# Performance work log

Measured on AMD Instinct MI355X. Metric: run time of the kernel, lower is better.

## Reference

```python
import jax, jax.numpy as jnp
import numpy as np

N_ROWS = 4_194_304  # batch rows
N_LAYERS = 30


def setup_inputs() -> dict:
    key = jax.random.key(0)
    k1, k2, k3, k4, k5 = jax.random.split(key, 5)
    x1 = jax.random.normal(k1, (N_ROWS, 1), dtype=jnp.float32)
    x2 = jax.random.normal(k2, (N_ROWS, 5), dtype=jnp.float32)
    # Per-layer params stacked: Linear(5->1) weight [1,5] + bias [1]; Linear(1->5, no bias) weight [5,1]
    W1 = jax.random.normal(k3, (N_LAYERS, 1, 5), dtype=jnp.float32) * (1.0 / np.sqrt(5.0))
    b1 = jax.random.normal(k4, (N_LAYERS, 1), dtype=jnp.float32) * (1.0 / np.sqrt(5.0))
    W2 = jax.random.normal(k5, (N_LAYERS, 5, 1), dtype=jnp.float32)
    return {"x1": x1, "x2": x2, "W1": W1, "b1": b1, "W2": W2}


def reference(x1, x2, W1, b1, W2):
    # Chain of 30 UpDownDoubleResNetBlock blocks:
    #   x1 = x1 + relu(x2) @ W1^T + b1   (Linear(5,1) with bias)
    #   x2 = x2 + relu(x1) @ W2^T        (Linear(1,5) no bias)
    def step(carry, params):
        h1, h2 = carry
        w1, bb1, w2 = params  # [1,5], [1], [5,1]
        h1 = h1 + jax.nn.relu(h2) @ w1.T + bb1  # [N,1]
        h2 = h2 + jax.nn.relu(h1) @ w2.T        # [N,5]
        return (h1, h2), None

    (x1, x2), _ = jax.lax.scan(step, (x1, x2), (W1, b1, W2))
    return (x1, x2)
```

## Files before the change

### kernel.cpp

```cpp
#include <hip/hip_runtime.h>

#define NL 30
#define RPB 512

typedef float v2f __attribute__((ext_vector_type(2)));

__global__ __launch_bounds__(256) void drn_kernel(
    const float* __restrict__ x1, const float* __restrict__ x2,
    const float* __restrict__ W1, const float* __restrict__ b1,
    const float* __restrict__ W2,
    float* __restrict__ o1, float* __restrict__ o2)
{
    __shared__ __align__(16) float slab[RPB * 5];

    const int t = threadIdx.x;
    const int base = blockIdx.x * RPB;

    const v2f* g2 = (const v2f*)(x2 + (size_t)base * 5);
    v2f* s2 = (v2f*)slab;
    #pragma unroll
    for (int k = 0; k < 5; ++k)
        s2[t + 256 * k] = g2[t + 256 * k];

    float h1x = x1[base + t];
    float h1y = x1[base + 256 + t];

    __syncthreads();

    float h2x[5], h2y[5];
    #pragma unroll
    for (int j = 0; j < 5; ++j) {
        h2x[j] = slab[5 * t + j];
        h2y[j] = slab[5 * t + 1280 + j];
    }

    #pragma unroll
    for (int l = 0; l < NL; ++l) {
        const float w10 = W1[l * 5 + 0], w11 = W1[l * 5 + 1], w12 = W1[l * 5 + 2],
                    w13 = W1[l * 5 + 3], w14 = W1[l * 5 + 4];
        const float bb  = b1[l];
        const float w20 = W2[l * 5 + 0], w21 = W2[l * 5 + 1], w22 = W2[l * 5 + 2],
                    w23 = W2[l * 5 + 3], w24 = W2[l * 5 + 4];

        {
            float s = h1x + bb;
            s = fmaf(fmaxf(h2x[0], 0.f), w10, s);
            s = fmaf(fmaxf(h2x[1], 0.f), w11, s);
            s = fmaf(fmaxf(h2x[2], 0.f), w12, s);
            s = fmaf(fmaxf(h2x[3], 0.f), w13, s);
            s = fmaf(fmaxf(h2x[4], 0.f), w14, s);
            h1x = s;
            const float rh = fmaxf(s, 0.f);
            h2x[0] = fmaf(rh, w20, h2x[0]);
            h2x[1] = fmaf(rh, w21, h2x[1]);
            h2x[2] = fmaf(rh, w22, h2x[2]);
            h2x[3] = fmaf(rh, w23, h2x[3]);
            h2x[4] = fmaf(rh, w24, h2x[4]);
        }
        {
            float s = h1y + bb;
            s = fmaf(fmaxf(h2y[0], 0.f), w10, s);
            s = fmaf(fmaxf(h2y[1], 0.f), w11, s);
            s = fmaf(fmaxf(h2y[2], 0.f), w12, s);
            s = fmaf(fmaxf(h2y[3], 0.f), w13, s);
            s = fmaf(fmaxf(h2y[4], 0.f), w14, s);
            h1y = s;
            const float rh = fmaxf(s, 0.f);
            h2y[0] = fmaf(rh, w20, h2y[0]);
            h2y[1] = fmaf(rh, w21, h2y[1]);
            h2y[2] = fmaf(rh, w22, h2y[2]);
            h2y[3] = fmaf(rh, w23, h2y[3]);
            h2y[4] = fmaf(rh, w24, h2y[4]);
        }
    }

    __builtin_nontemporal_store(h1x, &o1[base + t]);
    __builtin_nontemporal_store(h1y, &o1[base + 256 + t]);

    __syncthreads();
    #pragma unroll
    for (int j = 0; j < 5; ++j) {
        slab[5 * t + j]        = h2x[j];
        slab[5 * t + 1280 + j] = h2y[j];
    }
    __syncthreads();
    v2f* go2 = (v2f*)(o2 + (size_t)base * 5);
    #pragma unroll
    for (int k = 0; k < 5; ++k)
        __builtin_nontemporal_store(s2[t + 256 * k], &go2[t + 256 * k]);
}

extern "C" void kernel_launch(void* const* d_in, const int* in_sizes, int n_in,
                              void* d_out, int out_size, void* d_ws, size_t ws_size,
                              hipStream_t stream) {
    const float* x1 = (const float*)d_in[0];
    const float* x2 = (const float*)d_in[1];
    const float* W1 = (const float*)d_in[2];
    const float* b1 = (const float*)d_in[3];
    const float* W2 = (const float*)d_in[4];
    int nrows = in_sizes[0];
    float* o1 = (float*)d_out;
    float* o2 = (float*)d_out + nrows;

    int block = 256;
    int grid = nrows / RPB;
    drn_kernel<<<grid, block, 0, stream>>>(x1, x2, W1, b1, W2, o1, o2);
}
```

Before: 188.8 us.

## Use persistent per-wave tiles with register prefetch of the next tile

Replaces one-shot 512-row blocks with a fixed grid of 2048 blocks in which each wave owns a private LDS section and loops over 128-row tiles. The next tile's x1/x2 loads are issued into registers before the current tile's 30-layer compute, so global load latency overlaps the arithmetic, and block-wide __syncthreads is dropped in favour of wave-local compiler fences. This trades more register pressure and reliance on intra-wave LDS ordering for fewer block launches and better latency hiding.

```diff
diff --git a/kernel.cpp b/kernel.cpp
--- a/kernel.cpp
+++ b/kernel.cpp
@@ -1,93 +1,119 @@
 #include <hip/hip_runtime.h>
 
 #define NL 30
-#define RPB 512
+#define NBLK 2048
+#define NWAVES (NBLK * 4)
 
 typedef float v2f __attribute__((ext_vector_type(2)));
 
-__global__ __launch_bounds__(256) void drn_kernel(
+#define LDS_FENCE() asm volatile("" ::: "memory")
+
+__global__ __launch_bounds__(256, 8) void drn_kernel(
     const float* __restrict__ x1, const float* __restrict__ x2,
     const float* __restrict__ W1, const float* __restrict__ b1,
     const float* __restrict__ W2,
-    float* __restrict__ o1, float* __restrict__ o2)
+    float* __restrict__ o1, float* __restrict__ o2, int ntiles)
 {
-    __shared__ __align__(16) float slab[RPB * 5];
+    __shared__ __align__(16) float slab[4 * 640];
 
-    const int t = threadIdx.x;
-    const int base = blockIdx.x * RPB;
+    const int lane = threadIdx.x & 63;
+    const int w    = threadIdx.x >> 6;
+    float* sect  = &slab[w * 640];
+    v2f*   sect2 = (v2f*)sect;
 
-    const v2f* g2 = (const v2f*)(x2 + (size_t)base * 5);
-    v2f* s2 = (v2f*)slab;
+    const v2f* g2  = (const v2f*)x2;
+    v2f*       go2 = (v2f*)o2;
+
+    int tile = blockIdx.x * 4 + w;
+    if (tile >= ntiles) return;
+
+    v2f L[5];
     #pragma unroll
-    for (int k = 0; k < 5; ++k)
-        s2[t + 256 * k] = g2[t + 256 * k];
+    for (int k = 0; k < 5; ++k) L[k] = g2[(size_t)tile * 320 + lane + 64 * k];
+    float h1xn = x1[tile * 128 + lane];
+    float h1yn = x1[tile * 128 + 64 + lane];
 
-    float h1x = x1[base + t];
-    float h1y = x1[base + 256 + t];
+    while (true) {
+        LDS_FENCE();
+        #pragma unroll
+        for (int k = 0; k < 5; ++k) sect2[lane + 64 * k] = L[k];
+        const float h1x0 = h1xn, h1y0 = h1yn;
 
-    __syncthreads();
+        LDS_FENCE();
+        float h2x[5], h2y[5];
+        #pragma unroll
+        for (int j = 0; j < 5; ++j) {
+            h2x[j] = sect[5 * lane + j];
+            h2y[j] = sect[320 + 5 * lane + j];
+        }
 
-    float h2x[5], h2y[5];
-    #pragma unroll
-    for (int j = 0; j < 5; ++j) {
-        h2x[j] = slab[5 * t + j];
-        h2y[j] = slab[5 * t + 1280 + j];
+        const int ntile = tile + NWAVES;
+        const bool have_next = ntile < ntiles;
+        if (have_next) {
+            #pragma unroll
+            for (int k = 0; k < 5; ++k) L[k] = g2[(size_t)ntile * 320 + lane + 64 * k];
+            h1xn = x1[ntile * 128 + lane];
+            h1yn = x1[ntile * 128 + 64 + lane];
+        }
+
+        float h1x = h1x0, h1y = h1y0;
+        #pragma unroll
+        for (int l = 0; l < NL; ++l) {
+            const float w10 = W1[l*5+0], w11 = W1[l*5+1], w12 = W1[l*5+2],
+                        w13 = W1[l*5+3], w14 = W1[l*5+4];
+            const float bb  = b1[l];
+            const float w20 = W2[l*5+0], w21 = W2[l*5+1], w22 = W2[l*5+2],
+                        w23 = W2[l*5+3], w24 = W2[l*5+4];
+            {
+                float s = h1x + bb;
+                s = fmaf(fmaxf(h2x[0], 0.f), w10, s);
+                s = fmaf(fmaxf(h2x[1], 0.f), w11, s);
+                s = fmaf(fmaxf(h2x[2], 0.f), w12, s);
+                s = fmaf(fmaxf(h2x[3], 0.f), w13, s);
+                s = fmaf(fmaxf(h2x[4], 0.f), w14, s);
+                h1x = s;
+                const float rh = fmaxf(s, 0.f);
+                h2x[0] = fmaf(rh, w20, h2x[0]);
+                h2x[1] = fmaf(rh, w21, h2x[1]);
+                h2x[2] = fmaf(rh, w22, h2x[2]);
+                h2x[3] = fmaf(rh, w23, h2x[3]);
+                h2x[4] = fmaf(rh, w24, h2x[4]);
+            }
+            {
+                float s = h1y + bb;
+                s = fmaf(fmaxf(h2y[0], 0.f), w10, s);
+                s = fmaf(fmaxf(h2y[1], 0.f), w11, s);
+                s = fmaf(fmaxf(h2y[2], 0.f), w12, s);
+                s = fmaf(fmaxf(h2y[3], 0.f), w13, s);
+                s = fmaf(fmaxf(h2y[4], 0.f), w14, s);
+                h1y = s;
+                const float rh = fmaxf(s, 0.f);
+                h2y[0] = fmaf(rh, w20, h2y[0]);
+                h2y[1] = fmaf(rh, w21, h2y[1]);
+                h2y[2] = fmaf(rh, w22, h2y[2]);
+                h2y[3] = fmaf(rh, w23, h2y[3]);
+                h2y[4] = fmaf(rh, w24, h2y[4]);
+            }
+        }
+
+        __builtin_nontemporal_store(h1x, &o1[tile * 128 + lane]);
+        __builtin_nontemporal_store(h1y, &o1[tile * 128 + 64 + lane]);
+
+        LDS_FENCE();
+        #pragma unroll
+        for (int j = 0; j < 5; ++j) {
+            sect[5 * lane + j]       = h2x[j];
+            sect[320 + 5 * lane + j] = h2y[j];
+        }
+        LDS_FENCE();
+        #pragma unroll
+        for (int k = 0; k < 5; ++k)
+            __builtin_nontemporal_store(sect2[lane + 64 * k],
+                                        &go2[(size_t)tile * 320 + lane + 64 * k]);
+
+        if (!have_next) break;
+        tile = ntile;
     }
-
-    #pragma unroll
-    for (int l = 0; l < NL; ++l) {
-        const float w10 = W1[l * 5 + 0], w11 = W1[l * 5 + 1], w12 = W1[l * 5 + 2],
-                    w13 = W1[l * 5 + 3], w14 = W1[l * 5 + 4];
-        const float bb  = b1[l];
-        const float w20 = W2[l * 5 + 0], w21 = W2[l * 5 + 1], w22 = W2[l * 5 + 2],
-                    w23 = W2[l * 5 + 3], w24 = W2[l * 5 + 4];
-
-        {
-            float s = h1x + bb;
-            s = fmaf(fmaxf(h2x[0], 0.f), w10, s);
-            s = fmaf(fmaxf(h2x[1], 0.f), w11, s);
-            s = fmaf(fmaxf(h2x[2], 0.f), w12, s);
-            s = fmaf(fmaxf(h2x[3], 0.f), w13, s);
-            s = fmaf(fmaxf(h2x[4], 0.f), w14, s);
-            h1x = s;
-            const float rh = fmaxf(s, 0.f);
-            h2x[0] = fmaf(rh, w20, h2x[0]);
-            h2x[1] = fmaf(rh, w21, h2x[1]);
-            h2x[2] = fmaf(rh, w22, h2x[2]);
-            h2x[3] = fmaf(rh, w23, h2x[3]);
-            h2x[4] = fmaf(rh, w24, h2x[4]);
-        }
-        {
-            float s = h1y + bb;
-            s = fmaf(fmaxf(h2y[0], 0.f), w10, s);
-            s = fmaf(fmaxf(h2y[1], 0.f), w11, s);
-            s = fmaf(fmaxf(h2y[2], 0.f), w12, s);
-            s = fmaf(fmaxf(h2y[3], 0.f), w13, s);
-            s = fmaf(fmaxf(h2y[4], 0.f), w14, s);
-            h1y = s;
-            const float rh = fmaxf(s, 0.f);
-            h2y[0] = fmaf(rh, w20, h2y[0]);
-            h2y[1] = fmaf(rh, w21, h2y[1]);
-            h2y[2] = fmaf(rh, w22, h2y[2]);
-            h2y[3] = fmaf(rh, w23, h2y[3]);
-            h2y[4] = fmaf(rh, w24, h2y[4]);
-        }
-    }
-
-    __builtin_nontemporal_store(h1x, &o1[base + t]);
-    __builtin_nontemporal_store(h1y, &o1[base + 256 + t]);
-
-    __syncthreads();
-    #pragma unroll
-    for (int j = 0; j < 5; ++j) {
-        slab[5 * t + j]        = h2x[j];
-        slab[5 * t + 1280 + j] = h2y[j];
-    }
-    __syncthreads();
-    v2f* go2 = (v2f*)(o2 + (size_t)base * 5);
-    #pragma unroll
-    for (int k = 0; k < 5; ++k)
-        __builtin_nontemporal_store(s2[t + 256 * k], &go2[t + 256 * k]);
 }
 
 extern "C" void kernel_launch(void* const* d_in, const int* in_sizes, int n_in,
@@ -102,7 +128,6 @@
     float* o1 = (float*)d_out;
     float* o2 = (float*)d_out + nrows;
 
-    int block = 256;
-    int grid = nrows / RPB;
-    drn_kernel<<<grid, block, 0, stream>>>(x1, x2, W1, b1, W2, o1, o2);
+    int ntiles = nrows / 128;
+    drn_kernel<<<NBLK, 256, 0, stream>>>(x1, x2, W1, b1, W2, o1, o2, ntiles);
 }
```

New measurement: 192.4 us. About the same (+1.9%).
